# Optimization experiments

Hardware: AMD Instinct MI355X
Metric: run time of the kernel (lower is better)

## Reference

```python
import jax, jax.numpy as jnp
import numpy as np

E = 8        # numExperts
D = 1024     # d_model
F = 4096     # expert hidden = 4*d_model
T = 8192     # total tokens (sum of expertFrequency)


def setup_inputs() -> dict:
    key = jax.random.key(0)
    k0, k1, k2, k3, k4 = jax.random.split(key, 5)
    expertOrderedInput = jax.random.normal(k0, (T, D), dtype=jnp.float32)
    # Static equal split so the split sizes are jit-compatible.
    expertFrequency = jnp.full((E,), T // E, dtype=jnp.int64)
    s1 = 1.0 / np.sqrt(D)
    s2 = 1.0 / np.sqrt(F)
    w1 = jax.random.normal(k1, (E, D, F), dtype=jnp.float32) * s1
    b1 = jnp.zeros((E, F), dtype=jnp.float32)
    w2 = jax.random.normal(k2, (E, F, D), dtype=jnp.float32) * s2
    b2 = jnp.zeros((E, D), dtype=jnp.float32)
    return {"expertOrderedInput": expertOrderedInput,
            "expertFrequency": expertFrequency,
            "w1": w1, "b1": b1, "w2": w2, "b2": b2}


def reference(expertOrderedInput, expertFrequency, w1, b1, w2, b2):
    # expertOrderedInput: [T, D], tokens pre-sorted by expert.
    # expertFrequency is equal per expert (T/E each), so the
    # split-loop-cat in the torch module is exactly a grouped GEMM.
    e = w1.shape[0]
    t = expertOrderedInput.shape[0]
    x = expertOrderedInput.reshape(e, t // e, -1)            # [E, T/E, D]
    h = jax.nn.gelu(jnp.einsum('etd,edf->etf', x, w1) + b1[:, None, :])
    y = jnp.einsum('etf,efd->etd', h, w2) + b2[:, None, :]   # [E, T/E, D]
    return y.reshape(t, -1)                                   # cat along dim 0
```

## Files before the change

### kernel.cpp

```cpp
#include <hip/hip_runtime.h>

#define E_ 8
#define D_ 1024
#define F_ 4096
#define T_ 8192

typedef unsigned short u16;
typedef short bf16x8 __attribute__((ext_vector_type(8)));
typedef float f32x4 __attribute__((ext_vector_type(4)));
typedef unsigned short u16x8 __attribute__((ext_vector_type(8)));

__device__ __forceinline__ u16 f2bf(float f) {
    unsigned u = __builtin_bit_cast(unsigned, f);
    u += 0x7fffu + ((u >> 16) & 1u);
    return (u16)(u >> 16);
}

__device__ __forceinline__ float gelu_tanh(float x) {
    const float k0 = 0.7978845608028654f;
    const float k1 = 0.044715f;
    float t = tanhf(k0 * (x + k1 * x * x * x));
    return 0.5f * x * (1.0f + t);
}

__device__ __forceinline__ void async16(const void* g, void* l) {
    __builtin_amdgcn_global_load_lds(
        (const __attribute__((address_space(1))) unsigned int*)g,
        (__attribute__((address_space(3))) unsigned int*)l, 16, 0, 0);
}

__global__ void cvt_x(const float* __restrict__ in, u16* __restrict__ out) {
    int i = blockIdx.x * 256 + threadIdx.x;
    const float4* in4 = (const float4*)in;
    float4 a = in4[2 * i], b = in4[2 * i + 1];
    u16x8 o;
    o[0] = f2bf(a.x); o[1] = f2bf(a.y); o[2] = f2bf(a.z); o[3] = f2bf(a.w);
    o[4] = f2bf(b.x); o[5] = f2bf(b.y); o[6] = f2bf(b.z); o[7] = f2bf(b.w);
    *(u16x8*)(out + (size_t)i * 8) = o;
}

__global__ void transpose_cvt(const float* __restrict__ src, u16* __restrict__ dst,
                              int R, int C) {
    __shared__ float tile[32][33];
    int e = blockIdx.z;
    src += (size_t)e * R * C;
    dst += (size_t)e * R * C;
    int c0 = blockIdx.x * 32, r0 = blockIdx.y * 32;
    int tx = threadIdx.x, ty = threadIdx.y;
#pragma unroll
    for (int i = 0; i < 4; ++i)
        tile[ty + i * 8][tx] = src[(size_t)(r0 + ty + i * 8) * C + c0 + tx];
    __syncthreads();
#pragma unroll
    for (int i = 0; i < 4; ++i)
        dst[(size_t)(c0 + ty + i * 8) * R + r0 + tx] = f2bf(tile[tx][ty + i * 8]);
}

template <int EPI>
__global__ __launch_bounds__(256, 2) void gemm_bt(
    const u16* __restrict__ A,
    const u16* __restrict__ Bt,
    const float* __restrict__ bias,
    void* __restrict__ Cv,
    int Mpe, int N, int K) {
    __shared__ u16 As[128 * 64];
    __shared__ u16 Bs[128 * 64];
    int e = blockIdx.z;
    A    += (size_t)e * Mpe * K;
    Bt   += (size_t)e * N * K;
    bias += (size_t)e * N;
    int n0 = blockIdx.x * 128;
    int m0 = blockIdx.y * 128;
    int tid = threadIdx.x;
    int w = tid >> 6, lane = tid & 63;
    int lr = lane & 15, lg = lane >> 4;
    int wr = w >> 1, wc = w & 1;

    f32x4 acc[4][4];
    const f32x4 zero = {0.f, 0.f, 0.f, 0.f};
#pragma unroll
    for (int i = 0; i < 4; ++i)
#pragma unroll
        for (int j = 0; j < 4; ++j) acc[i][j] = zero;

    int nK = K >> 6;
    for (int kt = 0; kt < nK; ++kt) {
        int kb = kt << 6;
#pragma unroll
        for (int i = 0; i < 4; ++i) {
            int chunk = w * 256 + i * 64 + lane;
            int row = chunk >> 3, c8 = chunk & 7;
            async16(A  + (size_t)(m0 + row) * K + kb + c8 * 8,
                    As + (size_t)(w * 256 + i * 64) * 8);
            async16(Bt + (size_t)(n0 + row) * K + kb + c8 * 8,
                    Bs + (size_t)(w * 256 + i * 64) * 8);
        }
        __syncthreads();

        const bf16x8* As8 = (const bf16x8*)As;
        const bf16x8* Bs8 = (const bf16x8*)Bs;
#pragma unroll
        for (int h = 0; h < 2; ++h) {
            bf16x8 a[4], b[4];
#pragma unroll
            for (int i = 0; i < 4; ++i)
                a[i] = As8[(size_t)(wr * 64 + i * 16 + lr) * 8 + h * 4 + lg];
#pragma unroll
            for (int j = 0; j < 4; ++j)
                b[j] = Bs8[(size_t)(wc * 64 + j * 16 + lr) * 8 + h * 4 + lg];
#pragma unroll
            for (int i = 0; i < 4; ++i)
#pragma unroll
                for (int j = 0; j < 4; ++j)
                    acc[i][j] = __builtin_amdgcn_mfma_f32_16x16x32_bf16(
                        a[i], b[j], acc[i][j], 0, 0, 0);
        }
        __syncthreads();
    }

    int mb = m0 + wr * 64, nb = n0 + wc * 64;
    if (EPI == 1) {
        u16* C = (u16*)Cv + (size_t)e * Mpe * N;
#pragma unroll
        for (int i = 0; i < 4; ++i) {
#pragma unroll
            for (int j = 0; j < 4; ++j) {
                int col = nb + j * 16 + lr;
                float bv = bias[col];
                int row = mb + i * 16 + lg * 4;
#pragma unroll
                for (int t = 0; t < 4; ++t) {
                    float v = acc[i][j][t] + bv;
                    C[(size_t)(row + t) * N + col] = f2bf(gelu_tanh(v));
                }
            }
        }
    } else {
        float* C = (float*)Cv + (size_t)e * Mpe * N;
#pragma unroll
        for (int i = 0; i < 4; ++i) {
#pragma unroll
            for (int j = 0; j < 4; ++j) {
                int col = nb + j * 16 + lr;
                float bv = bias[col];
                int row = mb + i * 16 + lg * 4;
#pragma unroll
                for (int t = 0; t < 4; ++t)
                    C[(size_t)(row + t) * N + col] = acc[i][j][t] + bv;
            }
        }
    }
}

extern "C" void kernel_launch(void* const* d_in, const int* in_sizes, int n_in,
                              void* d_out, int out_size, void* d_ws, size_t ws_size,
                              hipStream_t stream) {
    const float* X  = (const float*)d_in[0];
    const float* w1 = (const float*)d_in[2];
    const float* b1 = (const float*)d_in[3];
    const float* w2 = (const float*)d_in[4];
    const float* b2 = (const float*)d_in[5];
    float* out = (float*)d_out;

    const size_t XBF_B = (size_t)T_ * D_ * 2;
    const size_t WT_B  = (size_t)E_ * F_ * D_ * 2;
    const size_t H_B   = (size_t)T_ * F_ * 2;
    if (ws_size < XBF_B + WT_B + H_B) return;

    char* ws = (char*)d_ws;
    u16* Xbf = (u16*)ws;
    u16* Wt  = (u16*)(ws + XBF_B);
    u16* H   = (u16*)(ws + XBF_B + WT_B);

    cvt_x<<<dim3((T_ * D_) / 8 / 256), dim3(256), 0, stream>>>(X, Xbf);
    transpose_cvt<<<dim3(F_ / 32, D_ / 32, E_), dim3(32, 8), 0, stream>>>(w1, Wt, D_, F_);
    gemm_bt<1><<<dim3(F_ / 128, (T_ / E_) / 128, E_), dim3(256), 0, stream>>>(
        Xbf, Wt, b1, H, T_ / E_, F_, D_);
    transpose_cvt<<<dim3(D_ / 32, F_ / 32, E_), dim3(32, 8), 0, stream>>>(w2, Wt, F_, D_);
    gemm_bt<0><<<dim3(D_ / 128, (T_ / E_) / 128, E_), dim3(256), 0, stream>>>(
        H, Wt, b2, out, T_ / E_, D_, F_);
}
```

Before: 302.3 us.

## Replace grouped GEMM with 8-wave ping-pong pipelined kernel using larger tiles

Replaces the simple single-buffered 128x128 bf16 MFMA GEMM with a 512-thread kernel using 256-row tiles that double-buffers K-halves in LDS. Async global-to-LDS loads for upcoming tiles are interleaved with MFMA phases under explicit vmcnt waits, barriers and setprio. The goal is to hide memory latency and raise data reuse per block. In exchange it adds complex manual synchronisation, higher LDS use (which may limit occupancy) and fewer blocks for the second GEMM.

```diff
diff --git a/kernel.cpp b/kernel.cpp
--- a/kernel.cpp
+++ b/kernel.cpp
@@ -56,73 +56,169 @@
         dst[(size_t)(c0 + ty + i * 8) * R + r0 + tx] = f2bf(tile[tx][ty + i * 8]);
 }
 
-template <int EPI>
-__global__ __launch_bounds__(256, 2) void gemm_bt(
+template <int BN, int WM, int WN, int EPI>
+__global__ __launch_bounds__(512, 2) void gemm8p(
     const u16* __restrict__ A,
     const u16* __restrict__ Bt,
     const float* __restrict__ bias,
     void* __restrict__ Cv,
     int Mpe, int N, int K) {
-    __shared__ u16 As[128 * 64];
-    __shared__ u16 Bs[128 * 64];
-    int e = blockIdx.z;
+    constexpr int BM  = 256;
+    constexpr int LA  = 2;
+    constexpr int LB  = BN / 128;
+    constexpr int WTM = BM / WM;
+    constexpr int MFR = WTM / 16;
+    constexpr int AELEM = 4 * BM * 32;
+    __shared__ u16 lds[AELEM + 4 * BN * 32];
+
+    const int tid = threadIdx.x;
+    const int w = tid >> 6, lane = tid & 63;
+    const int lr = lane & 15, lg = lane >> 4;
+    const int wm = w / WN, wn = w % WN;
+
+    const int e = blockIdx.z;
     A    += (size_t)e * Mpe * K;
     Bt   += (size_t)e * N * K;
     bias += (size_t)e * N;
-    int n0 = blockIdx.x * 128;
-    int m0 = blockIdx.y * 128;
-    int tid = threadIdx.x;
-    int w = tid >> 6, lane = tid & 63;
-    int lr = lane & 15, lg = lane >> 4;
-    int wr = w >> 1, wc = w & 1;
-
-    f32x4 acc[4][4];
+    const int n0 = blockIdx.x * BN;
+    const int m0 = blockIdx.y * BM;
+    const int NT = K >> 6;
+
+    const char* gA[LA];
+    const char* gB[LB];
+    {
+        int kch = lane & 3;
+#pragma unroll
+        for (int i = 0; i < LA; ++i) {
+            int row = i * 128 + w * 16 + (lane >> 2);
+            gA[i] = (const char*)(A + (size_t)(m0 + row) * K + kch * 8);
+        }
+#pragma unroll
+        for (int i = 0; i < LB; ++i) {
+            int row = i * 128 + w * 16 + (lane >> 2);
+            gB[i] = (const char*)(Bt + (size_t)(n0 + row) * K + kch * 8);
+        }
+    }
+    char* ldsc = (char*)lds;
+
+    auto stageA = [&](int t, int h) {
+        size_t goff = (size_t)t * 128 + (size_t)h * 64;
+        unsigned dst = (unsigned)((((t & 1) * 2 + h) * (BM * 64)) + w * 1024);
+#pragma unroll
+        for (int i = 0; i < LA; ++i)
+            async16(gA[i] + goff, ldsc + dst + i * 8192);
+    };
+    auto stageB = [&](int t, int h) {
+        size_t goff = (size_t)t * 128 + (size_t)h * 64;
+        unsigned dst = (unsigned)(AELEM * 2 + (((t & 1) * 2 + h) * (BN * 64)) + w * 1024);
+#pragma unroll
+        for (int i = 0; i < LB; ++i)
+            async16(gB[i] + goff, ldsc + dst + i * 8192);
+    };
+
+    f32x4 acc[MFR][4];
     const f32x4 zero = {0.f, 0.f, 0.f, 0.f};
 #pragma unroll
-    for (int i = 0; i < 4; ++i)
+    for (int i = 0; i < MFR; ++i)
 #pragma unroll
         for (int j = 0; j < 4; ++j) acc[i][j] = zero;
 
-    int nK = K >> 6;
-    for (int kt = 0; kt < nK; ++kt) {
-        int kb = kt << 6;
-#pragma unroll
-        for (int i = 0; i < 4; ++i) {
-            int chunk = w * 256 + i * 64 + lane;
-            int row = chunk >> 3, c8 = chunk & 7;
-            async16(A  + (size_t)(m0 + row) * K + kb + c8 * 8,
-                    As + (size_t)(w * 256 + i * 64) * 8);
-            async16(Bt + (size_t)(n0 + row) * K + kb + c8 * 8,
-                    Bs + (size_t)(w * 256 + i * 64) * 8);
-        }
-        __syncthreads();
-
-        const bf16x8* As8 = (const bf16x8*)As;
-        const bf16x8* Bs8 = (const bf16x8*)Bs;
-#pragma unroll
-        for (int h = 0; h < 2; ++h) {
-            bf16x8 a[4], b[4];
-#pragma unroll
-            for (int i = 0; i < 4; ++i)
-                a[i] = As8[(size_t)(wr * 64 + i * 16 + lr) * 8 + h * 4 + lg];
-#pragma unroll
-            for (int j = 0; j < 4; ++j)
-                b[j] = Bs8[(size_t)(wc * 64 + j * 16 + lr) * 8 + h * 4 + lg];
-#pragma unroll
-            for (int i = 0; i < 4; ++i)
-#pragma unroll
-                for (int j = 0; j < 4; ++j)
-                    acc[i][j] = __builtin_amdgcn_mfma_f32_16x16x32_bf16(
-                        a[i], b[j], acc[i][j], 0, 0, 0);
-        }
-        __syncthreads();
+    stageA(0, 0); stageB(0, 0); stageA(0, 1); stageB(0, 1);
+    stageA(1, 0); stageB(1, 0);
+    if constexpr (LB == 2) asm volatile("s_waitcnt vmcnt(8)" ::: "memory");
+    else                   asm volatile("s_waitcnt vmcnt(6)" ::: "memory");
+    __builtin_amdgcn_s_barrier();
+    __builtin_amdgcn_sched_barrier(0);
+
+    const u16* SBbase = lds + AELEM;
+    bf16x8 a[MFR];
+
+    for (int c = 0; c < NT; ++c) {
+        const int bb = c & 1;
+        const u16* SA0 = lds    + (bb * 2 + 0) * (BM * 32);
+        const u16* SA1 = lds    + (bb * 2 + 1) * (BM * 32);
+        const u16* SB0 = SBbase + (bb * 2 + 0) * (BN * 32);
+        const u16* SB1 = SBbase + (bb * 2 + 1) * (BN * 32);
+        const bool stg1 = (c + 1 < NT);
+        const bool stg2 = (c + 2 < NT);
+        const bool tail = (c >= NT - 2);
+        const int arow = wm * WTM + lr;
+        const int brow = wn * 64 + lr;
+
+#pragma unroll
+        for (int i = 0; i < MFR; ++i)
+            a[i] = *(const bf16x8*)(SA0 + (arow + i * 16) * 32 + lg * 8);
+        bf16x8 b0 = *(const bf16x8*)(SB0 + (brow +  0) * 32 + lg * 8);
+        bf16x8 b1 = *(const bf16x8*)(SB0 + (brow + 16) * 32 + lg * 8);
+        if (stg1) stageA(c + 1, 1);
+        __builtin_amdgcn_s_barrier();
+        __builtin_amdgcn_s_setprio(1);
+#pragma unroll
+        for (int i = 0; i < MFR; ++i) {
+            acc[i][0] = __builtin_amdgcn_mfma_f32_16x16x32_bf16(a[i], b0, acc[i][0], 0, 0, 0);
+            acc[i][1] = __builtin_amdgcn_mfma_f32_16x16x32_bf16(a[i], b1, acc[i][1], 0, 0, 0);
+        }
+        __builtin_amdgcn_s_setprio(0);
+        __builtin_amdgcn_s_barrier();
+        __builtin_amdgcn_sched_barrier(0);
+
+        b0 = *(const bf16x8*)(SB0 + (brow + 32) * 32 + lg * 8);
+        b1 = *(const bf16x8*)(SB0 + (brow + 48) * 32 + lg * 8);
+        if (stg1) stageB(c + 1, 1);
+        __builtin_amdgcn_s_barrier();
+        __builtin_amdgcn_s_setprio(1);
+#pragma unroll
+        for (int i = 0; i < MFR; ++i) {
+            acc[i][2] = __builtin_amdgcn_mfma_f32_16x16x32_bf16(a[i], b0, acc[i][2], 0, 0, 0);
+            acc[i][3] = __builtin_amdgcn_mfma_f32_16x16x32_bf16(a[i], b1, acc[i][3], 0, 0, 0);
+        }
+        __builtin_amdgcn_s_setprio(0);
+        if (tail) asm volatile("s_waitcnt vmcnt(0)" ::: "memory");
+        else if constexpr (LB == 2) asm volatile("s_waitcnt vmcnt(8)" ::: "memory");
+        else                        asm volatile("s_waitcnt vmcnt(6)" ::: "memory");
+        __builtin_amdgcn_s_barrier();
+        __builtin_amdgcn_sched_barrier(0);
+
+#pragma unroll
+        for (int i = 0; i < MFR; ++i)
+            a[i] = *(const bf16x8*)(SA1 + (arow + i * 16) * 32 + lg * 8);
+        b0 = *(const bf16x8*)(SB1 + (brow +  0) * 32 + lg * 8);
+        b1 = *(const bf16x8*)(SB1 + (brow + 16) * 32 + lg * 8);
+        if (stg2) stageA(c + 2, 0);
+        __builtin_amdgcn_s_barrier();
+        __builtin_amdgcn_s_setprio(1);
+#pragma unroll
+        for (int i = 0; i < MFR; ++i) {
+            acc[i][0] = __builtin_amdgcn_mfma_f32_16x16x32_bf16(a[i], b0, acc[i][0], 0, 0, 0);
+            acc[i][1] = __builtin_amdgcn_mfma_f32_16x16x32_bf16(a[i], b1, acc[i][1], 0, 0, 0);
+        }
+        __builtin_amdgcn_s_setprio(0);
+        __builtin_amdgcn_s_barrier();
+        __builtin_amdgcn_sched_barrier(0);
+
+        b0 = *(const bf16x8*)(SB1 + (brow + 32) * 32 + lg * 8);
+        b1 = *(const bf16x8*)(SB1 + (brow + 48) * 32 + lg * 8);
+        if (stg2) stageB(c + 2, 0);
+        __builtin_amdgcn_s_barrier();
+        __builtin_amdgcn_s_setprio(1);
+#pragma unroll
+        for (int i = 0; i < MFR; ++i) {
+            acc[i][2] = __builtin_amdgcn_mfma_f32_16x16x32_bf16(a[i], b0, acc[i][2], 0, 0, 0);
+            acc[i][3] = __builtin_amdgcn_mfma_f32_16x16x32_bf16(a[i], b1, acc[i][3], 0, 0, 0);
+        }
+        __builtin_amdgcn_s_setprio(0);
+        if (tail) asm volatile("s_waitcnt vmcnt(0)" ::: "memory");
+        else if constexpr (LB == 2) asm volatile("s_waitcnt vmcnt(8)" ::: "memory");
+        else                        asm volatile("s_waitcnt vmcnt(6)" ::: "memory");
+        __builtin_amdgcn_s_barrier();
+        __builtin_amdgcn_sched_barrier(0);
     }
 
-    int mb = m0 + wr * 64, nb = n0 + wc * 64;
-    if (EPI == 1) {
+    const int mb = m0 + wm * WTM, nb = n0 + wn * 64;
+    if constexpr (EPI == 1) {
         u16* C = (u16*)Cv + (size_t)e * Mpe * N;
 #pragma unroll
-        for (int i = 0; i < 4; ++i) {
+        for (int i = 0; i < MFR; ++i) {
 #pragma unroll
             for (int j = 0; j < 4; ++j) {
                 int col = nb + j * 16 + lr;
@@ -138,7 +234,7 @@
     } else {
         float* C = (float*)Cv + (size_t)e * Mpe * N;
 #pragma unroll
-        for (int i = 0; i < 4; ++i) {
+        for (int i = 0; i < MFR; ++i) {
 #pragma unroll
             for (int j = 0; j < 4; ++j) {
                 int col = nb + j * 16 + lr;
@@ -174,9 +270,9 @@
 
     cvt_x<<<dim3((T_ * D_) / 8 / 256), dim3(256), 0, stream>>>(X, Xbf);
     transpose_cvt<<<dim3(F_ / 32, D_ / 32, E_), dim3(32, 8), 0, stream>>>(w1, Wt, D_, F_);
-    gemm_bt<1><<<dim3(F_ / 128, (T_ / E_) / 128, E_), dim3(256), 0, stream>>>(
+    gemm8p<256, 2, 4, 1><<<dim3(F_ / 256, (T_ / E_) / 256, E_), dim3(512), 0, stream>>>(
         Xbf, Wt, b1, H, T_ / E_, F_, D_);
     transpose_cvt<<<dim3(D_ / 32, F_ / 32, E_), dim3(32, 8), 0, stream>>>(w2, Wt, F_, D_);
-    gemm_bt<0><<<dim3(D_ / 128, (T_ / E_) / 128, E_), dim3(256), 0, stream>>>(
+    gemm8p<128, 4, 2, 0><<<dim3(D_ / 128, (T_ / E_) / 256, E_), dim3(512), 0, stream>>>(
         H, Wt, b2, out, T_ / E_, D_, F_);
 }
```

New measurement: 303.5 us. About the same (+0.4%).
